# Performance work log

Hardware: AMD Instinct MI355X
Metric: run time of the kernel (lower is better)

The kernel has to match this reference:

```python
import jax, jax.numpy as jnp
import numpy as np

B, N1, N2, D = 4, 4096, 4096, 128


def setup_inputs() -> dict:
    key = jax.random.key(0)
    k1, k2 = jax.random.split(key)
    x1 = jax.random.normal(k1, (B, N1, D), dtype=jnp.float32)
    x2 = jax.random.normal(k2, (B, N2, D), dtype=jnp.float32)
    return {"x1": x1, "x2": x2}


def reference(x1, x2):
    # torch.cdist(x2, x1, p=2.0): pairwise euclidean distances [B, N2, N1]
    # Expansion form: ||a||^2 + ||b||^2 - 2 a.b  (single GEMM, no [B,N2,N1,D] intermediate)
    sq2 = jnp.sum(x2 * x2, axis=-1)                      # [B, N2]
    sq1 = jnp.sum(x1 * x1, axis=-1)                      # [B, N1]
    inner = jnp.einsum('bnd,bmd->bnm', x2, x1)           # [B, N2, N1]
    sq = sq2[:, :, None] + sq1[:, None, :] - 2.0 * inner
    corr_mat = jnp.sqrt(jnp.maximum(sq, 0.0))            # clamp numerical negatives
    max_ind21 = jnp.argmin(corr_mat, axis=-1)            # [B, N2] nearest x1 for each x2
    max_ind12 = jnp.argmin(corr_mat, axis=-2)            # [B, N1] nearest x2 for each x1
    return (x1, x2, corr_mat, max_ind12, max_ind21)
```

## Files before the change

### kernel.cpp

```cpp
#include <hip/hip_runtime.h>
#include <stdint.h>
#include <stddef.h>

#define BB 4
#define NN 4096
#define DD 128

typedef _Float16 f16;
typedef _Float16 f16x8 __attribute__((ext_vector_type(8)));
typedef float f32x4 __attribute__((ext_vector_type(4)));

__device__ __forceinline__ void gl16(const f16* g, f16* l) {
  __builtin_amdgcn_global_load_lds(
      (const __attribute__((address_space(1))) unsigned int*)g,
      (__attribute__((address_space(3))) unsigned int*)l,
      16, 0, 0);
}

__device__ __forceinline__ float fast_sqrt(float x) {
  float r;
  asm("v_sqrt_f32 %0, %1" : "=v"(r) : "v"(x));
  return r;
}

__global__ __launch_bounds__(256) void prep_kernel(
    const float* __restrict__ x1, const float* __restrict__ x2,
    f16* __restrict__ x1h, f16* __restrict__ x1l,
    f16* __restrict__ x2h, f16* __restrict__ x2l,
    float* __restrict__ sq1, float* __restrict__ sq2,
    float* __restrict__ out)
{
  int gtid = blockIdx.x * blockDim.x + threadIdx.x;
  int gwave = gtid >> 6;
  int lane = gtid & 63;
  int sub = lane >> 3;
  int j = lane & 7;
  int row = gwave * 8 + sub;
  const float* src; f16* dh; f16* dl; float* sq; float* cpy; int r;
  if (row < BB * NN) {
    r = row; src = x1; dh = x1h; dl = x1l; sq = sq1; cpy = out;
  } else {
    r = row - BB * NN; src = x2; dh = x2h; dl = x2l; sq = sq2;
    cpy = out + (size_t)BB * NN * DD;
  }
  const float* p = src + (size_t)r * DD;
  float acc = 0.0f;
  #pragma unroll
  for (int i = 0; i < DD / 8; ++i) {
    int c = j + i * 8;
    float v = p[c];
    float s = v * v;
    acc = (i == 0) ? s : (acc + s);
    f16 h = (f16)v;
    f16 l = (f16)(v - (float)h);
    dh[(size_t)r * DD + c] = h;
    dl[(size_t)r * DD + c] = l;
    cpy[(size_t)r * DD + c] = v;
  }
  acc = acc + __shfl_xor(acc, 1);
  acc = acc + __shfl_xor(acc, 2);
  acc = acc + __shfl_xor(acc, 4);
  if (j == 0) sq[r] = acc;
}

__global__ __launch_bounds__(512, 4) void cdist_kernel(
    const f16* __restrict__ x1h, const f16* __restrict__ x1l,
    const f16* __restrict__ x2h, const f16* __restrict__ x2l,
    const float* __restrict__ sq1, const float* __restrict__ sq2,
    float* __restrict__ corr,
    float* __restrict__ p21v, int* __restrict__ p21i,
    float* __restrict__ p12v, int* __restrict__ p12i)
{
  __shared__ f16 Ah[2][128 * 32];
  __shared__ f16 Al[2][128 * 32];
  __shared__ f16 Bh[2][128 * 32];
  __shared__ f16 Bl[2][128 * 32];
  __shared__ float s1s[128];
  __shared__ float s2s[128];

  const int b = blockIdx.z;
  int lin = blockIdx.y * 32 + blockIdx.x;
  lin = (lin & 7) * 128 + (lin >> 3);
  const int sbx = lin & 31;
  const int sby = lin >> 5;
  const int bn1 = sbx * 128;
  const int bn2 = sby * 128;

  const int t = threadIdx.x;
  const int wid = t >> 6;
  const int lane = t & 63;
  const int wm = wid & 1;
  const int wn = wid >> 1;
  const int lr = lane & 15;
  const int lg = lane >> 4;

  const f16* gAh = x1h + (size_t)b * NN * DD;
  const f16* gAl = x1l + (size_t)b * NN * DD;
  const f16* gBh = x2h + (size_t)b * NN * DD;
  const f16* gBl = x2l + (size_t)b * NN * DD;

  if (t < 128) s1s[t] = sq1[(size_t)b * NN + bn1 + t];
  else if (t < 256) s2s[t - 128] = sq2[(size_t)b * NN + bn2 + (t - 128)];

  const int rowc = t >> 2;
  const int kc = (t & 3) ^ (rowc & 3) ^ ((rowc >> 2) & 3);
  const int aoff = bn1 * DD + rowc * DD + kc * 8;
  const int boff = bn2 * DD + rowc * DD + kc * 8;
  const int loff = (wid * 64) * 8;
#define STAGE(k0, bf) do { \
    gl16(gAh + aoff + (k0), &Ah[bf][loff]); \
    gl16(gAl + aoff + (k0), &Al[bf][loff]); \
    gl16(gBh + boff + (k0), &Bh[bf][loff]); \
    gl16(gBl + boff + (k0), &Bl[bf][loff]); } while (0)

  f32x4 acc[4][2];
  #pragma unroll
  for (int m = 0; m < 4; ++m)
    #pragma unroll
    for (int n = 0; n < 2; ++n)
      #pragma unroll
      for (int q = 0; q < 4; ++q) acc[m][n][q] = 0.0f;

  STAGE(0, 0);
  __syncthreads();

  const int lgx8 = (lg ^ (lr & 3) ^ ((lr >> 2) & 3)) * 8;
  const int offA0 = (wm * 64 + lr) * 32 + lgx8;
  const int offB0 = (wn * 32 + lr) * 32 + lgx8;

  #pragma unroll
  for (int it = 0; it < 4; ++it) {
    const int bf = it & 1;
    f16x8 fah[4], fal[4], fbh[2], fbl[2];
    #pragma unroll
    for (int m = 0; m < 4; ++m) {
      fah[m] = *(const f16x8*)&Ah[bf][offA0 + m * 512];
      fal[m] = *(const f16x8*)&Al[bf][offA0 + m * 512];
    }
    #pragma unroll
    for (int n = 0; n < 2; ++n) {
      fbh[n] = *(const f16x8*)&Bh[bf][offB0 + n * 512];
      fbl[n] = *(const f16x8*)&Bl[bf][offB0 + n * 512];
    }
    if (it < 3) STAGE((it + 1) * 32, (it + 1) & 1);
    #pragma unroll
    for (int m = 0; m < 4; ++m)
      #pragma unroll
      for (int n = 0; n < 2; ++n) {
        acc[m][n] = __builtin_amdgcn_mfma_f32_16x16x32_f16(fah[m], fbh[n], acc[m][n], 0, 0, 0);
        acc[m][n] = __builtin_amdgcn_mfma_f32_16x16x32_f16(fah[m], fbl[n], acc[m][n], 0, 0, 0);
        acc[m][n] = __builtin_amdgcn_mfma_f32_16x16x32_f16(fal[m], fbh[n], acc[m][n], 0, 0, 0);
      }
    if (it < 3) __syncthreads();
  }
#undef STAGE

  float s2r[2];
  #pragma unroll
  for (int n = 0; n < 2; ++n) s2r[n] = s2s[wn * 32 + n * 16 + lr];
  float s1r[4][4];
  #pragma unroll
  for (int m = 0; m < 4; ++m)
    #pragma unroll
    for (int q = 0; q < 4; ++q) s1r[m][q] = s1s[wm * 64 + m * 16 + lg * 4 + q];

  float v21[2]; int i21[2];
  #pragma unroll
  for (int n = 0; n < 2; ++n) { v21[n] = 3.4e38f; i21[n] = 0; }

  float* cbp = corr + (size_t)b * NN * NN;
  #pragma unroll
  for (int m = 0; m < 4; ++m) {
    const int n1b = wm * 64 + m * 16 + lg * 4;
    float v12[4]; int i12[4];
    #pragma unroll
    for (int q = 0; q < 4; ++q) { v12[q] = 3.4e38f; i12[q] = 0; }
    #pragma unroll
    for (int n = 0; n < 2; ++n) {
      const int n2l = wn * 32 + n * 16 + lr;
      f32x4 dv;
      float sqc[4];
      #pragma unroll
      for (int q = 0; q < 4; ++q) {
        const float sv = fmaxf(fmaf(-2.0f, acc[m][n][q], s1r[m][q] + s2r[n]), 0.0f);
        sqc[q] = sv;
        dv[q] = fast_sqrt(sv);
      }
      *(f32x4*)(cbp + (size_t)(bn2 + n2l) * NN + (bn1 + n1b)) = dv;
      #pragma unroll
      for (int q = 0; q < 4; ++q) {
        if (sqc[q] < v21[n]) { v21[n] = sqc[q]; i21[n] = bn1 + n1b + q; }
        if (sqc[q] < v12[q]) { v12[q] = sqc[q]; i12[q] = bn2 + n2l; }
      }
    }
    #pragma unroll
    for (int q = 0; q < 4; ++q) {
      float v = v12[q]; int idx = i12[q];
      #pragma unroll
      for (int mask = 1; mask < 16; mask <<= 1) {
        float ov = __shfl_xor(v, mask);
        int oi = __shfl_xor(idx, mask);
        if (ov < v || (ov == v && oi < idx)) { v = ov; idx = oi; }
      }
      if (lr == 0) {
        const int colg = bn1 + n1b + q;
        const size_t o = ((size_t)b * NN + colg) * 128 + (sby * 4 + wn);
        p12v[o] = v; p12i[o] = idx;
      }
    }
  }
  #pragma unroll
  for (int n = 0; n < 2; ++n) {
    float v = v21[n]; int idx = i21[n];
    #pragma unroll
    for (int mask = 16; mask < 64; mask <<= 1) {
      float ov = __shfl_xor(v, mask);
      int oi = __shfl_xor(idx, mask);
      if (ov < v || (ov == v && oi < idx)) { v = ov; idx = oi; }
    }
    if (lg == 0) {
      const int rowg = bn2 + wn * 32 + n * 16 + lr;
      const size_t o = ((size_t)b * NN + rowg) * 64 + (sbx * 2 + wm);
      p21v[o] = v; p21i[o] = idx;
    }
  }
}

__global__ __launch_bounds__(256) void argmin_reduce_kernel(
    const float* __restrict__ p21v, const int* __restrict__ p21i,
    const float* __restrict__ p12v, const int* __restrict__ p12i,
    float* __restrict__ out_i12, float* __restrict__ out_i21)
{
  int gtid = blockIdx.x * blockDim.x + threadIdx.x;
  int gwave = gtid >> 6;
  int lane = gtid & 63;
  float v; int idx; float* dst; int r;
  if (gwave < BB * NN) {
    r = gwave;
    v = p21v[(size_t)r * 64 + lane];
    idx = p21i[(size_t)r * 64 + lane];
    dst = out_i21;
  } else {
    r = gwave - BB * NN;
    v = p12v[(size_t)r * 128 + lane];
    idx = p12i[(size_t)r * 128 + lane];
    float v2 = p12v[(size_t)r * 128 + 64 + lane];
    int i2 = p12i[(size_t)r * 128 + 64 + lane];
    if (v2 < v || (v2 == v && i2 < idx)) { v = v2; idx = i2; }
    dst = out_i12;
  }
  #pragma unroll
  for (int mask = 1; mask < 64; mask <<= 1) {
    float ov = __shfl_xor(v, mask);
    int oi = __shfl_xor(idx, mask);
    if (ov < v || (ov == v && oi < idx)) { v = ov; idx = oi; }
  }
  if (lane == 0) dst[r] = (float)idx;
}

extern "C" void kernel_launch(void* const* d_in, const int* in_sizes, int n_in,
                              void* d_out, int out_size, void* d_ws, size_t ws_size,
                              hipStream_t stream) {
  (void)in_sizes; (void)n_in; (void)out_size; (void)ws_size;
  const float* x1 = (const float*)d_in[0];
  const float* x2 = (const float*)d_in[1];
  float* out = (float*)d_out;
  char* ws = (char*)d_ws;
  const size_t nd = (size_t)BB * NN * DD;
  const size_t bn = (size_t)BB * NN;

  f16* x1h = (f16*)(ws + 0 * nd * 2);
  f16* x1l = (f16*)(ws + 1 * nd * 2);
  f16* x2h = (f16*)(ws + 2 * nd * 2);
  f16* x2l = (f16*)(ws + 3 * nd * 2);
  float* sq1 = (float*)(ws + 4 * nd * 2);
  float* sq2 = (float*)(ws + 4 * nd * 2 + bn * 4);
  char* pbase = ws + 4 * nd * 2 + 2 * bn * 4;
  float* p21v = (float*)(pbase);
  int*   p21i = (int*)  (pbase + 1 * bn * 64 * 4);
  float* p12v = (float*)(pbase + 2 * bn * 64 * 4);
  int*   p12i = (int*)  (pbase + 2 * bn * 64 * 4 + bn * 128 * 4);

  hipLaunchKernelGGL(prep_kernel, dim3(1024), dim3(256), 0, stream,
                     x1, x2, x1h, x1l, x2h, x2l, sq1, sq2, out);

  float* corr = out + 2 * nd;
  hipLaunchKernelGGL(cdist_kernel, dim3(32, 32, 4), dim3(512), 0, stream,
                     x1h, x1l, x2h, x2l, sq1, sq2, corr, p21v, p21i, p12v, p12i);

  float* out_i12 = out + 2 * nd + bn * (size_t)NN;
  float* out_i21 = out_i12 + bn;
  hipLaunchKernelGGL(argmin_reduce_kernel, dim3(8192), dim3(256), 0, stream,
                     p21v, p21i, p12v, p12i, out_i12, out_i21);
}
```

Measured before the change: 174.7 us.

## Stage output tile through LDS for coalesced nontemporal stores of distance matrix

Shared memory becomes one byte buffer with macro-addressed A/B staging regions. After the GEMM, the epilogue reuses that buffer to write the 128x128 fp32 distance tile with an XOR swizzle. Once every wave finishes writing, each wave reads back full rows and issues coalesced 512-byte row stores to corr using nontemporal hints. This targets the scattered 16-byte-per-row stores on the 256MB output, at the cost of an extra LDS round trip and two barriers, with 65KB LDS possibly limiting occupancy.

```diff
diff --git a/kernel.cpp b/kernel.cpp
--- a/kernel.cpp
+++ b/kernel.cpp
@@ -71,12 +71,14 @@
     float* __restrict__ p21v, int* __restrict__ p21i,
     float* __restrict__ p12v, int* __restrict__ p12i)
 {
-  __shared__ f16 Ah[2][128 * 32];
-  __shared__ f16 Al[2][128 * 32];
-  __shared__ f16 Bh[2][128 * 32];
-  __shared__ f16 Bl[2][128 * 32];
-  __shared__ float s1s[128];
-  __shared__ float s2s[128];
+  __shared__ __align__(16) char smem[66560];
+#define AH(bf) ((f16*)(smem + (bf) * 32768))
+#define AL(bf) ((f16*)(smem + (bf) * 32768 + 8192))
+#define BH(bf) ((f16*)(smem + (bf) * 32768 + 16384))
+#define BL(bf) ((f16*)(smem + (bf) * 32768 + 24576))
+  float* s1s = (float*)(smem + 65536);
+  float* s2s = (float*)(smem + 65536 + 512);
+  float* etile = (float*)smem;
 
   const int b = blockIdx.z;
   int lin = blockIdx.y * 32 + blockIdx.x;
@@ -108,10 +110,10 @@
   const int boff = bn2 * DD + rowc * DD + kc * 8;
   const int loff = (wid * 64) * 8;
 #define STAGE(k0, bf) do { \
-    gl16(gAh + aoff + (k0), &Ah[bf][loff]); \
-    gl16(gAl + aoff + (k0), &Al[bf][loff]); \
-    gl16(gBh + boff + (k0), &Bh[bf][loff]); \
-    gl16(gBl + boff + (k0), &Bl[bf][loff]); } while (0)
+    gl16(gAh + aoff + (k0), &AH(bf)[loff]); \
+    gl16(gAl + aoff + (k0), &AL(bf)[loff]); \
+    gl16(gBh + boff + (k0), &BH(bf)[loff]); \
+    gl16(gBl + boff + (k0), &BL(bf)[loff]); } while (0)
 
   f32x4 acc[4][2];
   #pragma unroll
@@ -134,13 +136,13 @@
     f16x8 fah[4], fal[4], fbh[2], fbl[2];
     #pragma unroll
     for (int m = 0; m < 4; ++m) {
-      fah[m] = *(const f16x8*)&Ah[bf][offA0 + m * 512];
-      fal[m] = *(const f16x8*)&Al[bf][offA0 + m * 512];
+      fah[m] = *(const f16x8*)&AH(bf)[offA0 + m * 512];
+      fal[m] = *(const f16x8*)&AL(bf)[offA0 + m * 512];
     }
     #pragma unroll
     for (int n = 0; n < 2; ++n) {
-      fbh[n] = *(const f16x8*)&Bh[bf][offB0 + n * 512];
-      fbl[n] = *(const f16x8*)&Bl[bf][offB0 + n * 512];
+      fbh[n] = *(const f16x8*)&BH(bf)[offB0 + n * 512];
+      fbl[n] = *(const f16x8*)&BL(bf)[offB0 + n * 512];
     }
     if (it < 3) STAGE((it + 1) * 32, (it + 1) & 1);
     #pragma unroll
@@ -164,20 +166,22 @@
     #pragma unroll
     for (int q = 0; q < 4; ++q) s1r[m][q] = s1s[wm * 64 + m * 16 + lg * 4 + q];
 
+  __syncthreads();
+
   float v21[2]; int i21[2];
   #pragma unroll
   for (int n = 0; n < 2; ++n) { v21[n] = 3.4e38f; i21[n] = 0; }
 
-  float* cbp = corr + (size_t)b * NN * NN;
   #pragma unroll
   for (int m = 0; m < 4; ++m) {
     const int n1b = wm * 64 + m * 16 + lg * 4;
+    const int slot = wm * 16 + m * 4 + lg;
     float v12[4]; int i12[4];
     #pragma unroll
     for (int q = 0; q < 4; ++q) { v12[q] = 3.4e38f; i12[q] = 0; }
     #pragma unroll
     for (int n = 0; n < 2; ++n) {
-      const int n2l = wn * 32 + n * 16 + lr;
+      const int row = wn * 32 + n * 16 + lr;
       f32x4 dv;
       float sqc[4];
       #pragma unroll
@@ -186,11 +190,11 @@
         sqc[q] = sv;
         dv[q] = fast_sqrt(sv);
       }
-      *(f32x4*)(cbp + (size_t)(bn2 + n2l) * NN + (bn1 + n1b)) = dv;
+      *(f32x4*)&etile[row * 128 + (slot ^ (lr & 7)) * 4] = dv;
       #pragma unroll
       for (int q = 0; q < 4; ++q) {
         if (sqc[q] < v21[n]) { v21[n] = sqc[q]; i21[n] = bn1 + n1b + q; }
-        if (sqc[q] < v12[q]) { v12[q] = sqc[q]; i12[q] = bn2 + n2l; }
+        if (sqc[q] < v12[q]) { v12[q] = sqc[q]; i12[q] = bn2 + row; }
       }
     }
     #pragma unroll
@@ -224,6 +228,22 @@
       p21v[o] = v; p21i[o] = idx;
     }
   }
+
+  __syncthreads();
+  float* cbp = corr + (size_t)b * NN * NN;
+  const int r2 = lane >> 5;
+  const int sl = lane & 31;
+  #pragma unroll
+  for (int p = 0; p < 8; ++p) {
+    const int row = wid * 16 + p * 2 + r2;
+    const f32x4 val = *(const f32x4*)&etile[row * 128 + (sl ^ (row & 7)) * 4];
+    __builtin_nontemporal_store(val,
+        (f32x4*)(cbp + (size_t)(bn2 + row) * NN + bn1 + sl * 4));
+  }
+#undef AH
+#undef AL
+#undef BH
+#undef BL
 }
 
 __global__ __launch_bounds__(256) void argmin_reduce_kernel(
```

Measured after the change: 168.2 us. 3.7% less time.

## Make cdist kernel persistent with cross-tile prefetch overlapping corr stores

Applied to the files above, without the earlier changes.

Replaces the 4096-block grid with 512 persistent blocks, each handling 8 output tiles mapped by XCD. The next tile's operands and norm vectors are prefetched into LDS during the current tile's epilogue, and corr stores are deferred until after that prefetch is issued, so global loads overlap the store stream. Synchronisation now uses manual s_waitcnt counts and sched_barriers. This lowers launch overhead and pipeline bubbles but depends on exact vmcnt accounting and holds more registers for the buffered dv tile.

```diff
diff --git a/kernel.cpp b/kernel.cpp
--- a/kernel.cpp
+++ b/kernel.cpp
@@ -10,7 +10,17 @@
 typedef _Float16 f16x8 __attribute__((ext_vector_type(8)));
 typedef float f32x4 __attribute__((ext_vector_type(4)));
 
+#define WAITV(N) asm volatile("s_waitcnt vmcnt(" #N ")" ::: "memory")
+#define WAITL0() asm volatile("s_waitcnt lgkmcnt(0)" ::: "memory")
+#define SCHED0() __builtin_amdgcn_sched_barrier(0)
+
 __device__ __forceinline__ void gl16(const f16* g, f16* l) {
+  __builtin_amdgcn_global_load_lds(
+      (const __attribute__((address_space(1))) unsigned int*)g,
+      (__attribute__((address_space(3))) unsigned int*)l,
+      16, 0, 0);
+}
+__device__ __forceinline__ void gl16f(const float* g, float* l) {
   __builtin_amdgcn_global_load_lds(
       (const __attribute__((address_space(1))) unsigned int*)g,
       (__attribute__((address_space(3))) unsigned int*)l,
@@ -78,13 +88,9 @@
   __shared__ float s1s[128];
   __shared__ float s2s[128];
 
-  const int b = blockIdx.z;
-  int lin = blockIdx.y * 32 + blockIdx.x;
-  lin = (lin & 7) * 128 + (lin >> 3);
-  const int sbx = lin & 31;
-  const int sby = lin >> 5;
-  const int bn1 = sbx * 128;
-  const int bn2 = sby * 128;
+  const int blk = blockIdx.x;
+  const int xcd = blk & 7;
+  const int slot = blk >> 3;
 
   const int t = threadIdx.x;
   const int wid = t >> 6;
@@ -94,136 +100,198 @@
   const int lr = lane & 15;
   const int lg = lane >> 4;
 
-  const f16* gAh = x1h + (size_t)b * NN * DD;
-  const f16* gAl = x1l + (size_t)b * NN * DD;
-  const f16* gBh = x2h + (size_t)b * NN * DD;
-  const f16* gBl = x2l + (size_t)b * NN * DD;
-
-  if (t < 128) s1s[t] = sq1[(size_t)b * NN + bn1 + t];
-  else if (t < 256) s2s[t - 128] = sq2[(size_t)b * NN + bn2 + (t - 128)];
-
   const int rowc = t >> 2;
-  const int kc = (t & 3) ^ (rowc & 3) ^ ((rowc >> 2) & 3);
-  const int aoff = bn1 * DD + rowc * DD + kc * 8;
-  const int boff = bn2 * DD + rowc * DD + kc * 8;
+  const int kc8 = ((t & 3) ^ (rowc & 3) ^ ((rowc >> 2) & 3)) * 8;
   const int loff = (wid * 64) * 8;
-#define STAGE(k0, bf) do { \
-    gl16(gAh + aoff + (k0), &Ah[bf][loff]); \
-    gl16(gAl + aoff + (k0), &Al[bf][loff]); \
-    gl16(gBh + boff + (k0), &Bh[bf][loff]); \
-    gl16(gBl + boff + (k0), &Bl[bf][loff]); } while (0)
-
-  f32x4 acc[4][2];
-  #pragma unroll
-  for (int m = 0; m < 4; ++m)
-    #pragma unroll
-    for (int n = 0; n < 2; ++n)
-      #pragma unroll
-      for (int q = 0; q < 4; ++q) acc[m][n][q] = 0.0f;
-
-  STAGE(0, 0);
-  __syncthreads();
-
   const int lgx8 = (lg ^ (lr & 3) ^ ((lr >> 2) & 3)) * 8;
   const int offA0 = (wm * 64 + lr) * 32 + lgx8;
   const int offB0 = (wn * 32 + lr) * 32 + lgx8;
 
-  #pragma unroll
-  for (int it = 0; it < 4; ++it) {
-    const int bf = it & 1;
-    f16x8 fah[4], fal[4], fbh[2], fbl[2];
+#define GEOM(ti, b_, bn1_, bn2_) \
+    int lin_##ti = xcd * 128 + ((ti) & 1) * 64 + slot; \
+    b_ = (ti) >> 1; bn1_ = (lin_##ti & 31) * 128; bn2_ = (lin_##ti >> 5) * 128;
+
+#define BOUNDARY(b_, bn1_, bn2_) do { \
+    if (lane < 32) { \
+      gl16f(sq1 + (size_t)(b_) * NN + (bn1_) + lane * 4, s1s); \
+      gl16f(sq2 + (size_t)(b_) * NN + (bn2_) + lane * 4, s2s); \
+    } \
+    SCHED0(); \
+    const size_t base_ = (size_t)(b_) * NN * DD; \
+    const int ao_ = (bn1_ + rowc) * DD + kc8; \
+    const int bo_ = (bn2_ + rowc) * DD + kc8; \
+    gl16(x1h + base_ + ao_, &Ah[0][loff]); \
+    gl16(x1l + base_ + ao_, &Al[0][loff]); \
+    gl16(x2h + base_ + bo_, &Bh[0][loff]); \
+    gl16(x2l + base_ + bo_, &Bl[0][loff]); \
+    SCHED0(); \
+    gl16(x1h + base_ + ao_ + 32, &Ah[1][loff]); \
+    gl16(x1l + base_ + ao_ + 32, &Al[1][loff]); \
+    gl16(x2h + base_ + bo_ + 32, &Bh[1][loff]); \
+    gl16(x2l + base_ + bo_ + 32, &Bl[1][loff]); \
+    SCHED0(); } while (0)
+
+  {
+    int b0, bn10, bn20;
+    GEOM(0, b0, bn10, bn20);
+    BOUNDARY(b0, bn10, bn20);
+  }
+
+  for (int ti = 0; ti < 8; ++ti) {
+    int b, bn1, bn2;
+    GEOM(ti, b, bn1, bn2);
+    const size_t base = (size_t)b * NN * DD;
+    const int ao = (bn1 + rowc) * DD + kc8;
+    const int bo = (bn2 + rowc) * DD + kc8;
+
+    f32x4 acc[4][2];
+    #pragma unroll
+    for (int m = 0; m < 4; ++m)
+      #pragma unroll
+      for (int n = 0; n < 2; ++n)
+        #pragma unroll
+        for (int q = 0; q < 4; ++q) acc[m][n][q] = 0.0f;
+
+    #pragma unroll
+    for (int k = 0; k < 4; ++k) {
+      WAITL0(); SCHED0();
+      if (ti == 0) { if (k == 0) WAITV(4); else WAITV(0); }
+      else { if (k == 0) WAITV(12); else if (k == 1) WAITV(8); else WAITV(0); }
+      __builtin_amdgcn_s_barrier();
+      SCHED0();
+      if (k == 1) {
+        gl16(x1h + base + ao + 64, &Ah[0][loff]);
+        gl16(x1l + base + ao + 64, &Al[0][loff]);
+        gl16(x2h + base + bo + 64, &Bh[0][loff]);
+        gl16(x2l + base + bo + 64, &Bl[0][loff]);
+      }
+      if (k == 2) {
+        gl16(x1h + base + ao + 96, &Ah[1][loff]);
+        gl16(x1l + base + ao + 96, &Al[1][loff]);
+        gl16(x2h + base + bo + 96, &Bh[1][loff]);
+        gl16(x2l + base + bo + 96, &Bl[1][loff]);
+      }
+      SCHED0();
+      const int bf = k & 1;
+      f16x8 fah[4], fal[4], fbh[2], fbl[2];
+      #pragma unroll
+      for (int m = 0; m < 4; ++m) {
+        fah[m] = *(const f16x8*)&Ah[bf][offA0 + m * 512];
+        fal[m] = *(const f16x8*)&Al[bf][offA0 + m * 512];
+      }
+      #pragma unroll
+      for (int n = 0; n < 2; ++n) {
+        fbh[n] = *(const f16x8*)&Bh[bf][offB0 + n * 512];
+        fbl[n] = *(const f16x8*)&Bl[bf][offB0 + n * 512];
+      }
+      #pragma unroll
+      for (int m = 0; m < 4; ++m)
+        #pragma unroll
+        for (int n = 0; n < 2; ++n) {
+          acc[m][n] = __builtin_amdgcn_mfma_f32_16x16x32_f16(fah[m], fbh[n], acc[m][n], 0, 0, 0);
+          acc[m][n] = __builtin_amdgcn_mfma_f32_16x16x32_f16(fah[m], fbl[n], acc[m][n], 0, 0, 0);
+          acc[m][n] = __builtin_amdgcn_mfma_f32_16x16x32_f16(fal[m], fbh[n], acc[m][n], 0, 0, 0);
+        }
+    }
+
+    float s2r[2];
+    #pragma unroll
+    for (int n = 0; n < 2; ++n) s2r[n] = s2s[wn * 32 + n * 16 + lr];
+    float s1r[4][4];
+    #pragma unroll
+    for (int m = 0; m < 4; ++m)
+      #pragma unroll
+      for (int q = 0; q < 4; ++q) s1r[m][q] = s1s[wm * 64 + m * 16 + lg * 4 + q];
+
+    f32x4 dv[4][2];
+    float v21[2]; int i21[2];
+    #pragma unroll
+    for (int n = 0; n < 2; ++n) { v21[n] = 3.4e38f; i21[n] = 0; }
+
+    const int sbx = bn1 >> 7;
+    const int sby = bn2 >> 7;
     #pragma unroll
     for (int m = 0; m < 4; ++m) {
-      fah[m] = *(const f16x8*)&Ah[bf][offA0 + m * 512];
-      fal[m] = *(const f16x8*)&Al[bf][offA0 + m * 512];
+      const int n1b = wm * 64 + m * 16 + lg * 4;
+      float v12[4]; int i12[4];
+      #pragma unroll
+      for (int q = 0; q < 4; ++q) { v12[q] = 3.4e38f; i12[q] = 0; }
+      #pragma unroll
+      for (int n = 0; n < 2; ++n) {
+        float sqc[4];
+        #pragma unroll
+        for (int q = 0; q < 4; ++q) {
+          const float sv = fmaxf(fmaf(-2.0f, acc[m][n][q], s1r[m][q] + s2r[n]), 0.0f);
+          sqc[q] = sv;
+          dv[m][n][q] = fast_sqrt(sv);
+        }
+        const int n2l = wn * 32 + n * 16 + lr;
+        #pragma unroll
+        for (int q = 0; q < 4; ++q) {
+          if (sqc[q] < v21[n]) { v21[n] = sqc[q]; i21[n] = bn1 + n1b + q; }
+          if (sqc[q] < v12[q]) { v12[q] = sqc[q]; i12[q] = bn2 + n2l; }
+        }
+      }
+      #pragma unroll
+      for (int q = 0; q < 4; ++q) {
+        float v = v12[q]; int idx = i12[q];
+        #pragma unroll
+        for (int mask = 1; mask < 16; mask <<= 1) {
+          float ov = __shfl_xor(v, mask);
+          int oi = __shfl_xor(idx, mask);
+          if (ov < v || (ov == v && oi < idx)) { v = ov; idx = oi; }
+        }
+        if (lr == 0) {
+          const int colg = bn1 + n1b + q;
+          const size_t o = ((size_t)b * NN + colg) * 128 + (sby * 4 + wn);
+          p12v[o] = v; p12i[o] = idx;
+        }
+      }
     }
     #pragma unroll
     for (int n = 0; n < 2; ++n) {
-      fbh[n] = *(const f16x8*)&Bh[bf][offB0 + n * 512];
-      fbl[n] = *(const f16x8*)&Bl[bf][offB0 + n * 512];
-    }
-    if (it < 3) STAGE((it + 1) * 32, (it + 1) & 1);
-    #pragma unroll
-    for (int m = 0; m < 4; ++m)
-      #pragma unroll
-      for (int n = 0; n < 2; ++n) {
-        acc[m][n] = __builtin_amdgcn_mfma_f32_16x16x32_f16(fah[m], fbh[n], acc[m][n], 0, 0, 0);
-        acc[m][n] = __builtin_amdgcn_mfma_f32_16x16x32_f16(fah[m], fbl[n], acc[m][n], 0, 0, 0);
-        acc[m][n] = __builtin_amdgcn_mfma_f32_16x16x32_f16(fal[m], fbh[n], acc[m][n], 0, 0, 0);
-      }
-    if (it < 3) __syncthreads();
-  }
-#undef STAGE
-
-  float s2r[2];
-  #pragma unroll
-  for (int n = 0; n < 2; ++n) s2r[n] = s2s[wn * 32 + n * 16 + lr];
-  float s1r[4][4];
-  #pragma unroll
-  for (int m = 0; m < 4; ++m)
-    #pragma unroll
-    for (int q = 0; q < 4; ++q) s1r[m][q] = s1s[wm * 64 + m * 16 + lg * 4 + q];
-
-  float v21[2]; int i21[2];
-  #pragma unroll
-  for (int n = 0; n < 2; ++n) { v21[n] = 3.4e38f; i21[n] = 0; }
-
-  float* cbp = corr + (size_t)b * NN * NN;
-  #pragma unroll
-  for (int m = 0; m < 4; ++m) {
-    const int n1b = wm * 64 + m * 16 + lg * 4;
-    float v12[4]; int i12[4];
-    #pragma unroll
-    for (int q = 0; q < 4; ++q) { v12[q] = 3.4e38f; i12[q] = 0; }
-    #pragma unroll
-    for (int n = 0; n < 2; ++n) {
-      const int n2l = wn * 32 + n * 16 + lr;
-      f32x4 dv;
-      float sqc[4];
-      #pragma unroll
-      for (int q = 0; q < 4; ++q) {
-        const float sv = fmaxf(fmaf(-2.0f, acc[m][n][q], s1r[m][q] + s2r[n]), 0.0f);
-        sqc[q] = sv;
-        dv[q] = fast_sqrt(sv);
-      }
-      *(f32x4*)(cbp + (size_t)(bn2 + n2l) * NN + (bn1 + n1b)) = dv;
-      #pragma unroll
-      for (int q = 0; q < 4; ++q) {
-        if (sqc[q] < v21[n]) { v21[n] = sqc[q]; i21[n] = bn1 + n1b + q; }
-        if (sqc[q] < v12[q]) { v12[q] = sqc[q]; i12[q] = bn2 + n2l; }
-      }
-    }
-    #pragma unroll
-    for (int q = 0; q < 4; ++q) {
-      float v = v12[q]; int idx = i12[q];
-      #pragma unroll
-      for (int mask = 1; mask < 16; mask <<= 1) {
+      float v = v21[n]; int idx = i21[n];
+      #pragma unroll
+      for (int mask = 16; mask < 64; mask <<= 1) {
         float ov = __shfl_xor(v, mask);
         int oi = __shfl_xor(idx, mask);
         if (ov < v || (ov == v && oi < idx)) { v = ov; idx = oi; }
       }
-      if (lr == 0) {
-        const int colg = bn1 + n1b + q;
-        const size_t o = ((size_t)b * NN + colg) * 128 + (sby * 4 + wn);
-        p12v[o] = v; p12i[o] = idx;
-      }
-    }
-  }
-  #pragma unroll
-  for (int n = 0; n < 2; ++n) {
-    float v = v21[n]; int idx = i21[n];
-    #pragma unroll
-    for (int mask = 16; mask < 64; mask <<= 1) {
-      float ov = __shfl_xor(v, mask);
-      int oi = __shfl_xor(idx, mask);
-      if (ov < v || (ov == v && oi < idx)) { v = ov; idx = oi; }
-    }
-    if (lg == 0) {
-      const int rowg = bn2 + wn * 32 + n * 16 + lr;
-      const size_t o = ((size_t)b * NN + rowg) * 64 + (sbx * 2 + wm);
-      p21v[o] = v; p21i[o] = idx;
-    }
-  }
+      if (lg == 0) {
+        const int rowg = bn2 + wn * 32 + n * 16 + lr;
+        const size_t o = ((size_t)b * NN + rowg) * 64 + (sbx * 2 + wm);
+        p21v[o] = v; p21i[o] = idx;
+      }
+    }
+
+    WAITL0(); SCHED0();
+    __builtin_amdgcn_s_barrier();
+    SCHED0();
+    if (ti < 7) {
+      int bN, bn1N, bn2N;
+      if (ti == 0) { GEOM(1, bN, bn1N, bn2N); BOUNDARY(bN, bn1N, bn2N); }
+      else if (ti == 1) { GEOM(2, bN, bn1N, bn2N); BOUNDARY(bN, bn1N, bn2N); }
+      else if (ti == 2) { GEOM(3, bN, bn1N, bn2N); BOUNDARY(bN, bn1N, bn2N); }
+      else if (ti == 3) { GEOM(4, bN, bn1N, bn2N); BOUNDARY(bN, bn1N, bn2N); }
+      else if (ti == 4) { GEOM(5, bN, bn1N, bn2N); BOUNDARY(bN, bn1N, bn2N); }
+      else if (ti == 5) { GEOM(6, bN, bn1N, bn2N); BOUNDARY(bN, bn1N, bn2N); }
+      else { GEOM(7, bN, bn1N, bn2N); BOUNDARY(bN, bn1N, bn2N); }
+    }
+    SCHED0();
+    float* cbp = corr + (size_t)b * NN * NN;
+    #pragma unroll
+    for (int m = 0; m < 4; ++m) {
+      const int n1b = wm * 64 + m * 16 + lg * 4;
+      #pragma unroll
+      for (int n = 0; n < 2; ++n) {
+        const int n2g = bn2 + wn * 32 + n * 16 + lr;
+        *(f32x4*)(cbp + (size_t)n2g * NN + (bn1 + n1b)) = dv[m][n];
+      }
+    }
+    SCHED0();
+  }
+#undef BOUNDARY
+#undef GEOM
 }
 
 __global__ __launch_bounds__(256) void argmin_reduce_kernel(
@@ -285,7 +353,7 @@
                      x1, x2, x1h, x1l, x2h, x2l, sq1, sq2, out);
 
   float* corr = out + 2 * nd;
-  hipLaunchKernelGGL(cdist_kernel, dim3(32, 32, 4), dim3(512), 0, stream,
+  hipLaunchKernelGGL(cdist_kernel, dim3(512), dim3(512), 0, stream,
                      x1h, x1l, x2h, x2l, sq1, sq2, corr, p21v, p21i, p12v, p12i);
 
   float* out_i12 = out + 2 * nd + bn * (size_t)NN;
```

New measurement: 251.0 us. +43.7%, slower.
